# Kernel tuning notes

Measured on AMD Instinct MI355X. Metric: run time of the kernel, lower is better.

The kernel has to match this reference:

```python
import jax, jax.numpy as jnp
import numpy as np

N_NODES = 50000
N_EDGES = 800000
D_IN, D_HID, D_LAT = 128, 128, 64
BN_EPS = 1e-5


def setup_inputs() -> dict:
    key = jax.random.key(0)
    ks = jax.random.split(key, 8)
    x = jax.random.normal(ks[0], (N_NODES, D_IN), dtype=jnp.float32)
    edge_index = jax.random.randint(ks[1], (2, N_EDGES), 0, N_NODES, dtype=jnp.int64)
    s1 = 1.0 / np.sqrt(D_IN)
    s2 = 1.0 / np.sqrt(D_HID)
    W1 = jax.random.normal(ks[2], (D_IN, D_HID), dtype=jnp.float32) * s1
    b1 = jnp.zeros((D_HID,), jnp.float32)
    gamma = jnp.ones((D_HID,), jnp.float32)
    beta = jnp.zeros((D_HID,), jnp.float32)
    Wmu = jax.random.normal(ks[3], (D_HID, D_LAT), dtype=jnp.float32) * s2
    bmu = jnp.zeros((D_LAT,), jnp.float32)
    Wls = jax.random.normal(ks[4], (D_HID, D_LAT), dtype=jnp.float32) * s2
    bls = jnp.zeros((D_LAT,), jnp.float32)
    return {"x": x, "edge_index": edge_index, "W1": W1, "b1": b1,
            "gamma": gamma, "beta": beta, "Wmu": Wmu, "bmu": bmu,
            "Wls": Wls, "bls": bls}


def _gcn_conv(h, src, dst, norm_e, inv_deg, W, b):
    # PyG GCNConv: linear transform, then sym-normalized aggregation (A+I).
    h = h @ W                                   # [N, F]
    msgs = h[src] * norm_e[:, None]             # gather + edge scaling, [E, F]
    agg = jax.ops.segment_sum(msgs, dst, num_segments=h.shape[0])
    # self-loop contribution: norm[i]*norm[i] = 1/deg[i]
    return agg + h * inv_deg[:, None] + b


def reference(x, edge_index, W1, b1, gamma, beta, Wmu, bmu, Wls, bls):
    src, dst = edge_index[0], edge_index[1]
    n = x.shape[0]
    # degrees including self loops (GCN symmetric normalization)
    deg = jax.ops.segment_sum(jnp.ones(dst.shape, x.dtype), dst, num_segments=n) + 1.0
    inv_sqrt_deg = jax.lax.rsqrt(deg)
    norm_e = inv_sqrt_deg[src] * inv_sqrt_deg[dst]   # per-edge norm, [E]
    inv_deg = 1.0 / deg

    h = _gcn_conv(x, src, dst, norm_e, inv_deg, W1, b1)
    # BatchNorm1d with batch statistics (biased var), then ReLU; dropout off (eval)
    mean = h.mean(axis=0)
    var = h.var(axis=0)
    h = (h - mean) * jax.lax.rsqrt(var + BN_EPS) * gamma + beta
    h = jax.nn.relu(h)

    mu = _gcn_conv(h, src, dst, norm_e, inv_deg, Wmu, bmu)
    log_std = _gcn_conv(h, src, dst, norm_e, inv_deg, Wls, bls)
    return mu, log_std
```

## Files before the change

kernel.cpp:

```cpp
#include <hip/hip_runtime.h>
#include <hip/hip_bf16.h>

#define N_NODES 50000
#define N_EDGES 800000
#define F 128
#define L 64
#define BN_EPS 1e-5f
#define SCAN_BLOCKS 196
#define BN_BLOCKS 391
#define EDGE_BLOCKS 3125
#define GEMM_BLOCKS 782
#define NPART 8
#define PART_SZ 6250
#define SUBS 158
#define FILLB 1264

typedef __attribute__((ext_vector_type(8))) short short8;
typedef __attribute__((ext_vector_type(8))) unsigned short ushort8;
typedef __attribute__((ext_vector_type(4))) unsigned short ushortx4;
typedef __attribute__((ext_vector_type(4))) float f32x4;

static __device__ __forceinline__ float loadF(const void* p, int i, int f32) {
    if (f32) return ((const float*)p)[i];
    return __bfloat162float(((const __hip_bfloat16*)p)[i]);
}
static __device__ __forceinline__ float bfu2f(unsigned short u) {
    unsigned int t = ((unsigned int)u) << 16;
    float f;
    __builtin_memcpy(&f, &t, 4);
    return f;
}
static __device__ __forceinline__ short f2bf_s(float f) {
    union { __hip_bfloat16 b; short s; } cv;
    cv.b = __float2bfloat16(f);
    return cv.s;
}
static __device__ __forceinline__ unsigned short f2bf_u(float f) {
    union { __hip_bfloat16 b; unsigned short u; } cv;
    cv.b = __float2bfloat16(f);
    return cv.u;
}

__global__ void k_prep(const void* __restrict__ W1, const void* __restrict__ Wmu,
                       const void* __restrict__ Wls, const unsigned short* __restrict__ xs,
                       const void* __restrict__ ei, __hip_bfloat16* __restrict__ Wt1,
                       __hip_bfloat16* __restrict__ Wt2, int* __restrict__ flags,
                       int* __restrict__ degi, int* __restrict__ src32,
                       int* __restrict__ dst32, int* __restrict__ rank) {
    int b = blockIdx.x;
    int t = threadIdx.x;
    if (b == 0) {
        __shared__ int cnt[2];
        if (t < 2) cnt[t] = 0;
        __syncthreads();
        unsigned short v = xs[2 * t];
        int e = (v >> 7) & 0xff;
        int sane = (e >= 112 && e <= 133) ? 1 : 0;
        if (v == 0 || v == 0x8000) sane = 1;
        atomicAdd(&cnt[0], sane);
        atomicAdd(&cnt[1], (((const int*)ei)[2 * t + 1] != 0) ? 1 : 0);
        __syncthreads();
        if (t == 0) {
            flags[0] = (cnt[0] < 128) ? 1 : 0;
            flags[1] = (cnt[1] < 8) ? 1 : 0;
            flags[2] = 0;
        }
    } else if (b <= 64) {
        __shared__ int cnt;
        if (t == 0) cnt = 0;
        __syncthreads();
        unsigned short v = ((const unsigned short*)W1)[2 * t];
        int e = (v >> 7) & 0xff;
        atomicAdd(&cnt, (e >= 100 && e <= 133) ? 1 : 0);
        __syncthreads();
        int f32 = (cnt < 128) ? 1 : 0;
        int idx = (b - 1) * 256 + t;
        int n = idx >> 7, k = idx & 127;
        Wt1[idx] = __float2bfloat16(loadF(W1, k * F + n, f32));
        float v2 = (n < L) ? loadF(Wmu, k * L + n, f32) : loadF(Wls, k * L + (n - L), f32);
        Wt2[idx] = __float2bfloat16(v2);
    } else {
        int e0 = (b - 65) * 256 + t;
        __shared__ int nz;
        if (t == 0) nz = 0;
        __syncthreads();
        int w = ((const int*)ei)[2 * e0 + 1];
        if (w != 0) atomicAdd(&nz, 1);
        __syncthreads();
        int d;
        if (nz < 8) {
            int s = (int)((const long long*)ei)[e0];
            d = (int)((const long long*)ei)[N_EDGES + e0];
            src32[e0] = s;
            dst32[e0] = d;
        } else {
            d = ((const int*)ei)[N_EDGES + e0];
        }
        rank[e0] = atomicAdd(&degi[d], 1);
    }
}

__global__ void k_offs_alloc(const int* __restrict__ degi, int* __restrict__ flags,
                             int* __restrict__ offs, float* __restrict__ isd) {
    __shared__ int s[256];
    __shared__ int base;
    int t = threadIdx.x;
    int i = blockIdx.x * 256 + t;
    int v = (i < N_NODES) ? degi[i] : 0;
    s[t] = v;
    __syncthreads();
    for (int o = 1; o < 256; o <<= 1) {
        int u = (t >= o) ? s[t - o] : 0;
        __syncthreads();
        s[t] += u;
        __syncthreads();
    }
    if (t == 255) base = atomicAdd(&flags[2], s[255]);
    __syncthreads();
    if (i < N_NODES) {
        offs[i] = base + s[t] - v;
        isd[i] = 1.0f / sqrtf((float)v + 1.0f);
    }
}

static __device__ __forceinline__ void gemm_body(int bid, const void* __restrict__ Xin,
        const __hip_bfloat16* __restrict__ Wt, const float* __restrict__ isd,
        const int* __restrict__ flags, int mode,
        const float* __restrict__ bnscale, const float* __restrict__ bnshift,
        unsigned short* __restrict__ outb) {
    int wave = threadIdx.x >> 6, lane = threadIdx.x & 63;
    int quad = lane >> 4, mr = lane & 15;
    int m0 = bid * 64 + wave * 16;
    int node = m0 + mr;
    int row = (node < N_NODES) ? node : N_NODES - 1;
    short8 a[4];
    if (mode == 1) {
        const unsigned short* xb = (const unsigned short*)Xin;
#pragma unroll
        for (int t = 0; t < 4; ++t) {
            int k0 = t * 32 + quad * 8;
            ushort8 raw = *(const ushort8*)(xb + row * F + k0);
            f32x4 s0 = *(const f32x4*)(bnscale + k0);
            f32x4 s1 = *(const f32x4*)(bnscale + k0 + 4);
            f32x4 h0 = *(const f32x4*)(bnshift + k0);
            f32x4 h1 = *(const f32x4*)(bnshift + k0 + 4);
            short8 av;
#pragma unroll
            for (int j = 0; j < 4; ++j)
                av[j] = f2bf_s(fmaxf(bfu2f(raw[j]) * s0[j] + h0[j], 0.f));
#pragma unroll
            for (int j = 0; j < 4; ++j)
                av[4 + j] = f2bf_s(fmaxf(bfu2f(raw[4 + j]) * s1[j] + h1[j], 0.f));
            a[t] = av;
        }
    } else if (flags[0]) {
        const float* xf = (const float*)Xin;
#pragma unroll
        for (int t = 0; t < 4; ++t) {
            int off = row * F + t * 32 + quad * 8;
            f32x4 v0 = *(const f32x4*)(xf + off);
            f32x4 v1 = *(const f32x4*)(xf + off + 4);
            short8 av;
#pragma unroll
            for (int j = 0; j < 4; ++j) av[j] = f2bf_s(v0[j]);
#pragma unroll
            for (int j = 0; j < 4; ++j) av[4 + j] = f2bf_s(v1[j]);
            a[t] = av;
        }
    } else {
        const short* xb = (const short*)Xin;
#pragma unroll
        for (int t = 0; t < 4; ++t)
            a[t] = *(const short8*)(xb + row * F + t * 32 + quad * 8);
    }
    f32x4 acc[8];
    const short* wb = (const short*)Wt;
#pragma unroll
    for (int nt = 0; nt < 8; ++nt) {
        const short* wp = wb + (nt * 16 + mr) * F + quad * 8;
        f32x4 c = {0.f, 0.f, 0.f, 0.f};
        c = __builtin_amdgcn_mfma_f32_16x16x32_bf16(*(const short8*)(wp), a[0], c, 0, 0, 0);
        c = __builtin_amdgcn_mfma_f32_16x16x32_bf16(*(const short8*)(wp + 32), a[1], c, 0, 0, 0);
        c = __builtin_amdgcn_mfma_f32_16x16x32_bf16(*(const short8*)(wp + 64), a[2], c, 0, 0, 0);
        c = __builtin_amdgcn_mfma_f32_16x16x32_bf16(*(const short8*)(wp + 96), a[3], c, 0, 0, 0);
        acc[nt] = c;
    }
    if (node < N_NODES) {
        float sd = isd[node];
        unsigned short* op = outb + node * F;
#pragma unroll
        for (int nt = 0; nt < 8; ++nt) {
            ushortx4 r;
#pragma unroll
            for (int j = 0; j < 4; ++j) r[j] = f2bf_u(acc[nt][j] * sd);
            *(ushortx4*)(op + nt * 16 + quad * 4) = r;
        }
    }
}

__global__ __launch_bounds__(256) void k_fill_gemm1(
        const int* __restrict__ ei32, const int* __restrict__ src32,
        const int* __restrict__ dst32, const int* __restrict__ rank,
        const int* __restrict__ flags, const int* __restrict__ offs,
        int* __restrict__ csr,
        const void* __restrict__ X, const __hip_bfloat16* __restrict__ Wt1,
        const float* __restrict__ isd, unsigned short* __restrict__ outb) {
    if (blockIdx.x < GEMM_BLOCKS) {
        gemm_body(blockIdx.x, X, Wt1, isd, flags, 0, nullptr, nullptr, outb);
    } else {
        const int* sp;
        const int* dp;
        if (flags[1]) { sp = src32; dp = dst32; }
        else          { sp = ei32;  dp = ei32 + N_EDGES; }
        int grp = blockIdx.x & (NPART - 1);
        int sub = (blockIdx.x - GEMM_BLOCKS) >> 3;
        int lo = grp * PART_SZ, hi = lo + PART_SZ;
        int stride = SUBS * 256;
        for (int e = sub * 256 + threadIdx.x; e < N_EDGES; e += stride) {
            int d = dp[e];
            if (d >= lo && d < hi) csr[offs[d] + rank[e]] = sp[e];
        }
    }
}

__global__ __launch_bounds__(256) void k_gemm_bn(const void* __restrict__ Xin,
        const __hip_bfloat16* __restrict__ Wt, const float* __restrict__ isd,
        const int* __restrict__ flags, const float* __restrict__ bnscale,
        const float* __restrict__ bnshift, unsigned short* __restrict__ outb) {
    gemm_body(blockIdx.x, Xin, Wt, isd, flags, 1, bnscale, bnshift, outb);
}

static __device__ __forceinline__ void agg_accum(int node, int grp, int l16,
        const ushort8* __restrict__ vp, const int* __restrict__ csr,
        const int* __restrict__ offs, const int* __restrict__ degi, float acc[8]) {
#pragma unroll
    for (int j = 0; j < 8; ++j) acc[j] = 0.f;
    if (grp == 0) {
        ushort8 u = vp[node * 16 + l16];
#pragma unroll
        for (int j = 0; j < 8; ++j) acc[j] = bfu2f(u[j]);
    }
    int start = offs[node];
    int end = start + degi[node];
    int i = start + grp;
    for (; i + 12 < end; i += 16) {
        ushort8 u0 = vp[csr[i] * 16 + l16];
        ushort8 u1 = vp[csr[i + 4] * 16 + l16];
        ushort8 u2 = vp[csr[i + 8] * 16 + l16];
        ushort8 u3 = vp[csr[i + 12] * 16 + l16];
#pragma unroll
        for (int j = 0; j < 8; ++j)
            acc[j] += (bfu2f(u0[j]) + bfu2f(u1[j])) + (bfu2f(u2[j]) + bfu2f(u3[j]));
    }
    for (; i + 4 < end; i += 8) {
        ushort8 u0 = vp[csr[i] * 16 + l16];
        ushort8 u1 = vp[csr[i + 4] * 16 + l16];
#pragma unroll
        for (int j = 0; j < 8; ++j) acc[j] += bfu2f(u0[j]) + bfu2f(u1[j]);
    }
    for (; i < end; i += 4) {
        ushort8 u = vp[csr[i] * 16 + l16];
#pragma unroll
        for (int j = 0; j < 8; ++j) acc[j] += bfu2f(u[j]);
    }
#pragma unroll
    for (int j = 0; j < 8; ++j) {
        acc[j] += __shfl_xor(acc[j], 16);
        acc[j] += __shfl_xor(acc[j], 32);
    }
}

__global__ void k_agg1(const unsigned short* __restrict__ val, const int* __restrict__ csr,
                       const int* __restrict__ offs, const int* __restrict__ degi,
                       const float* __restrict__ isd, const void* __restrict__ b1,
                       const int* __restrict__ flags, unsigned short* __restrict__ out) {
    int node = blockIdx.x * 4 + (threadIdx.x >> 6);
    if (node >= N_NODES) return;
    int lane = threadIdx.x & 63;
    int grp = lane >> 4, l16 = lane & 15;
    float acc[8];
    agg_accum(node, grp, l16, (const ushort8*)val, csr, offs, degi, acc);
    if (grp == 0) {
        float sd = isd[node];
        int c0 = l16 * 8, f32 = flags[0];
        ushort8 r;
#pragma unroll
        for (int j = 0; j < 8; ++j) r[j] = f2bf_u(acc[j] * sd + loadF(b1, c0 + j, f32));
        ((ushort8*)out)[node * 16 + l16] = r;
    }
}

__global__ void k_bnstats(const unsigned short* __restrict__ h, float* __restrict__ partial) {
    __shared__ float ls[256][8];
    __shared__ float lq[256][8];
    int t = threadIdx.x;
    int o = t & 15, rg = t >> 4;
    int row0 = blockIdx.x * 128 + rg;
    float s[8] = {0.f}, q[8] = {0.f};
#pragma unroll
    for (int i = 0; i < 8; ++i) {
        int row = row0 + i * 16;
        if (row < N_NODES) {
            ushort8 u = *(const ushort8*)(h + row * F + o * 8);
#pragma unroll
            for (int j = 0; j < 8; ++j) {
                float v = bfu2f(u[j]);
                s[j] += v;
                q[j] += v * v;
            }
        }
    }
#pragma unroll
    for (int j = 0; j < 8; ++j) { ls[t][j] = s[j]; lq[t][j] = q[j]; }
    __syncthreads();
    if (t < 128) {
        int c = t, oo = c >> 3, jj = c & 7;
        float ts = 0.f, tq = 0.f;
#pragma unroll
        for (int rgi = 0; rgi < 16; ++rgi) {
            ts += ls[rgi * 16 + oo][jj];
            tq += lq[rgi * 16 + oo][jj];
        }
        partial[blockIdx.x * 256 + c] = ts;
        partial[blockIdx.x * 256 + 128 + c] = tq;
    }
}

__global__ void k_bnredprep(const float* __restrict__ partial, const void* __restrict__ gamma,
                            const void* __restrict__ beta, const int* __restrict__ flags,
                            float* __restrict__ scale, float* __restrict__ shift) {
    int c = blockIdx.x;
    float s = 0.f, q = 0.f;
    for (int b = threadIdx.x; b < BN_BLOCKS; b += 256) {
        s += partial[b * 256 + c];
        q += partial[b * 256 + 128 + c];
    }
#pragma unroll
    for (int o = 32; o; o >>= 1) {
        s += __shfl_down(s, o);
        q += __shfl_down(q, o);
    }
    __shared__ float ws[4], wq[4];
    if ((threadIdx.x & 63) == 0) {
        ws[threadIdx.x >> 6] = s;
        wq[threadIdx.x >> 6] = q;
    }
    __syncthreads();
    if (threadIdx.x == 0) {
        float S = ws[0] + ws[1] + ws[2] + ws[3];
        float Q = wq[0] + wq[1] + wq[2] + wq[3];
        const float invN = 1.0f / (float)N_NODES;
        float m = S * invN;
        float var = Q * invN - m * m;
        int f32 = flags[0];
        float sc = loadF(gamma, c, f32) * rsqrtf(var + BN_EPS);
        scale[c] = sc;
        shift[c] = loadF(beta, c, f32) - m * sc;
    }
}

__global__ void k_agg2(const unsigned short* __restrict__ val, const int* __restrict__ csr,
                       const int* __restrict__ offs, const int* __restrict__ degi,
                       const float* __restrict__ isd, const void* __restrict__ bmu,
                       const void* __restrict__ bls, const int* __restrict__ flags,
                       void* __restrict__ out) {
    int node = blockIdx.x * 4 + (threadIdx.x >> 6);
    if (node >= N_NODES) return;
    int lane = threadIdx.x & 63;
    int grp = lane >> 4, l16 = lane & 15;
    float acc[8];
    agg_accum(node, grp, l16, (const ushort8*)val, csr, offs, degi, acc);
    if (grp == 0) {
        float sd = isd[node];
        int c0 = l16 * 8, f32 = flags[0];
        int hsel = (c0 >= L) ? 1 : 0;
        int cc = c0 - hsel * L;
        const void* bp = hsel ? bls : bmu;
        float o8[8];
#pragma unroll
        for (int j = 0; j < 8; ++j) o8[j] = acc[j] * sd + loadF(bp, cc + j, f32);
        long base_o = (long)hsel * (N_NODES * 64) + (long)node * 64 + cc;
        if (f32) {
            f32x4 r0 = {o8[0], o8[1], o8[2], o8[3]};
            f32x4 r1 = {o8[4], o8[5], o8[6], o8[7]};
            __builtin_nontemporal_store(r0, (f32x4*)((float*)out + base_o));
            __builtin_nontemporal_store(r1, (f32x4*)((float*)out + base_o + 4));
        } else {
            ushort8 r;
#pragma unroll
            for (int j = 0; j < 8; ++j) r[j] = f2bf_u(o8[j]);
            __builtin_nontemporal_store(r, (ushort8*)((__hip_bfloat16*)out + base_o));
        }
    }
}

extern "C" void kernel_launch(void* const* d_in, const int* in_sizes, int n_in,
                              void* d_out, int out_size, void* d_ws, size_t ws_size,
                              hipStream_t stream) {
    const void* x     = d_in[0];
    const void* ei    = d_in[1];
    const void* W1    = d_in[2];
    const void* b1    = d_in[3];
    const void* gamma = d_in[4];
    const void* beta  = d_in[5];
    const void* Wmu   = d_in[6];
    const void* bmu   = d_in[7];
    const void* Wls   = d_in[8];
    const void* bls   = d_in[9];

    int*   degi  = (int*)d_ws;
    int*   offs  = degi + 50048;
    float* isd   = (float*)(offs + 50048);
    float* stats = isd + 50048;
    int*   flags = (int*)(stats + 512);
    int*   csr   = flags + 16;
    int*   src32 = csr + 800000;
    int*   dst32 = src32 + 800000;
    int*   rank  = dst32 + 800000;
    __hip_bfloat16* Wt1 = (__hip_bfloat16*)(rank + 800000);
    __hip_bfloat16* Wt2 = Wt1 + 16384;
    unsigned short* Abf = (unsigned short*)(Wt2 + 16384);
    unsigned short* Hpre = Abf + N_NODES * F;
    float* partial = (float*)(Hpre + N_NODES * F);

    const int NT = 256;
    const int AGG_BLOCKS = (N_NODES + 3) / 4;

    hipMemsetAsync(degi, 0, 50048 * sizeof(int), stream);
    k_prep<<<65 + EDGE_BLOCKS, NT, 0, stream>>>(W1, Wmu, Wls, (const unsigned short*)x,
                                                ei, Wt1, Wt2, flags, degi, src32, dst32,
                                                rank);
    k_offs_alloc<<<SCAN_BLOCKS, NT, 0, stream>>>(degi, flags, offs, isd);
    k_fill_gemm1<<<GEMM_BLOCKS + FILLB, NT, 0, stream>>>(
        (const int*)ei, src32, dst32, rank, flags, offs, csr, x, Wt1, isd, Abf);
    k_agg1<<<AGG_BLOCKS, NT, 0, stream>>>(Abf, csr, offs, degi, isd, b1, flags, Hpre);
    k_bnstats<<<BN_BLOCKS, NT, 0, stream>>>(Hpre, partial);
    k_bnredprep<<<128, NT, 0, stream>>>(partial, gamma, beta, flags, stats, stats + 128);
    k_gemm_bn<<<GEMM_BLOCKS, NT, 0, stream>>>(Hpre, Wt2, isd, flags, stats, stats + 128, Abf);
    k_agg2<<<AGG_BLOCKS, NT, 0, stream>>>(Abf, csr, offs, degi, isd, bmu, bls, flags, d_out);
}
```

Baseline: 286.4 us.

## Overlap GEMM1 with edge degree counting by moving source normalization into aggregation

The first GEMM no longer scales its output rows by the source node's inverse sqrt degree. That lets it run in the same launch as edge degree counting instead of waiting for the degree scan. The per-source scale moves into the aggregation loops, which now load isd[src] for every gathered neighbour and multiply per element. The CSR fill becomes its own kernel with more blocks. The cost is an extra gather per edge in both aggregations, plus one more kernel launch.

```diff
diff --git a/kernel.cpp b/kernel.cpp
--- a/kernel.cpp
+++ b/kernel.cpp
@@ -12,8 +12,8 @@
 #define GEMM_BLOCKS 782
 #define NPART 8
 #define PART_SZ 6250
-#define SUBS 158
-#define FILLB 1264
+#define SUBS_F 256
+#define FILLB_A 2048
 
 typedef __attribute__((ext_vector_type(8))) short short8;
 typedef __attribute__((ext_vector_type(8))) unsigned short ushort8;
@@ -41,12 +41,10 @@
     return cv.u;
 }
 
-__global__ void k_prep(const void* __restrict__ W1, const void* __restrict__ Wmu,
-                       const void* __restrict__ Wls, const unsigned short* __restrict__ xs,
-                       const void* __restrict__ ei, __hip_bfloat16* __restrict__ Wt1,
-                       __hip_bfloat16* __restrict__ Wt2, int* __restrict__ flags,
-                       int* __restrict__ degi, int* __restrict__ src32,
-                       int* __restrict__ dst32, int* __restrict__ rank) {
+__global__ void k_wprep(const void* __restrict__ W1, const void* __restrict__ Wmu,
+                        const void* __restrict__ Wls, const unsigned short* __restrict__ xs,
+                        const void* __restrict__ ei, __hip_bfloat16* __restrict__ Wt1,
+                        __hip_bfloat16* __restrict__ Wt2, int* __restrict__ flags) {
     int b = blockIdx.x;
     int t = threadIdx.x;
     if (b == 0) {
@@ -65,7 +63,7 @@
             flags[1] = (cnt[1] < 8) ? 1 : 0;
             flags[2] = 0;
         }
-    } else if (b <= 64) {
+    } else {
         __shared__ int cnt;
         if (t == 0) cnt = 0;
         __syncthreads();
@@ -79,8 +77,92 @@
         Wt1[idx] = __float2bfloat16(loadF(W1, k * F + n, f32));
         float v2 = (n < L) ? loadF(Wmu, k * L + n, f32) : loadF(Wls, k * L + (n - L), f32);
         Wt2[idx] = __float2bfloat16(v2);
+    }
+}
+
+static __device__ __forceinline__ void gemm_body(int bid, const void* __restrict__ Xin,
+        const __hip_bfloat16* __restrict__ Wt, const int* __restrict__ flags, int mode,
+        const float* __restrict__ bnscale, const float* __restrict__ bnshift,
+        unsigned short* __restrict__ outb) {
+    int wave = threadIdx.x >> 6, lane = threadIdx.x & 63;
+    int quad = lane >> 4, mr = lane & 15;
+    int m0 = bid * 64 + wave * 16;
+    int node = m0 + mr;
+    int row = (node < N_NODES) ? node : N_NODES - 1;
+    short8 a[4];
+    if (mode == 1) {
+        const unsigned short* xb = (const unsigned short*)Xin;
+#pragma unroll
+        for (int t = 0; t < 4; ++t) {
+            int k0 = t * 32 + quad * 8;
+            ushort8 raw = *(const ushort8*)(xb + row * F + k0);
+            f32x4 s0 = *(const f32x4*)(bnscale + k0);
+            f32x4 s1 = *(const f32x4*)(bnscale + k0 + 4);
+            f32x4 h0 = *(const f32x4*)(bnshift + k0);
+            f32x4 h1 = *(const f32x4*)(bnshift + k0 + 4);
+            short8 av;
+#pragma unroll
+            for (int j = 0; j < 4; ++j)
+                av[j] = f2bf_s(fmaxf(bfu2f(raw[j]) * s0[j] + h0[j], 0.f));
+#pragma unroll
+            for (int j = 0; j < 4; ++j)
+                av[4 + j] = f2bf_s(fmaxf(bfu2f(raw[4 + j]) * s1[j] + h1[j], 0.f));
+            a[t] = av;
+        }
+    } else if (flags[0]) {
+        const float* xf = (const float*)Xin;
+#pragma unroll
+        for (int t = 0; t < 4; ++t) {
+            int off = row * F + t * 32 + quad * 8;
+            f32x4 v0 = *(const f32x4*)(xf + off);
+            f32x4 v1 = *(const f32x4*)(xf + off + 4);
+            short8 av;
+#pragma unroll
+            for (int j = 0; j < 4; ++j) av[j] = f2bf_s(v0[j]);
+#pragma unroll
+            for (int j = 0; j < 4; ++j) av[4 + j] = f2bf_s(v1[j]);
+            a[t] = av;
+        }
     } else {
-        int e0 = (b - 65) * 256 + t;
+        const short* xb = (const short*)Xin;
+#pragma unroll
+        for (int t = 0; t < 4; ++t)
+            a[t] = *(const short8*)(xb + row * F + t * 32 + quad * 8);
+    }
+    f32x4 acc[8];
+    const short* wb = (const short*)Wt;
+#pragma unroll
+    for (int nt = 0; nt < 8; ++nt) {
+        const short* wp = wb + (nt * 16 + mr) * F + quad * 8;
+        f32x4 c = {0.f, 0.f, 0.f, 0.f};
+        c = __builtin_amdgcn_mfma_f32_16x16x32_bf16(*(const short8*)(wp), a[0], c, 0, 0, 0);
+        c = __builtin_amdgcn_mfma_f32_16x16x32_bf16(*(const short8*)(wp + 32), a[1], c, 0, 0, 0);
+        c = __builtin_amdgcn_mfma_f32_16x16x32_bf16(*(const short8*)(wp + 64), a[2], c, 0, 0, 0);
+        c = __builtin_amdgcn_mfma_f32_16x16x32_bf16(*(const short8*)(wp + 96), a[3], c, 0, 0, 0);
+        acc[nt] = c;
+    }
+    if (node < N_NODES) {
+        unsigned short* op = outb + node * F;
+#pragma unroll
+        for (int nt = 0; nt < 8; ++nt) {
+            ushortx4 r;
+#pragma unroll
+            for (int j = 0; j < 4; ++j) r[j] = f2bf_u(acc[nt][j]);
+            *(ushortx4*)(op + nt * 16 + quad * 4) = r;
+        }
+    }
+}
+
+__global__ __launch_bounds__(256) void k_edge_gemm1(
+        const void* __restrict__ X, const __hip_bfloat16* __restrict__ Wt1,
+        const int* __restrict__ flags, const void* __restrict__ ei,
+        int* __restrict__ degi, int* __restrict__ src32, int* __restrict__ dst32,
+        int* __restrict__ rank, unsigned short* __restrict__ outb) {
+    if (blockIdx.x < GEMM_BLOCKS) {
+        gemm_body(blockIdx.x, X, Wt1, flags, 0, nullptr, nullptr, outb);
+    } else {
+        int t = threadIdx.x;
+        int e0 = (blockIdx.x - GEMM_BLOCKS) * 256 + t;
         __shared__ int nz;
         if (t == 0) nz = 0;
         __syncthreads();
@@ -123,145 +205,73 @@
     }
 }
 
-static __device__ __forceinline__ void gemm_body(int bid, const void* __restrict__ Xin,
-        const __hip_bfloat16* __restrict__ Wt, const float* __restrict__ isd,
-        const int* __restrict__ flags, int mode,
-        const float* __restrict__ bnscale, const float* __restrict__ bnshift,
-        unsigned short* __restrict__ outb) {
-    int wave = threadIdx.x >> 6, lane = threadIdx.x & 63;
-    int quad = lane >> 4, mr = lane & 15;
-    int m0 = bid * 64 + wave * 16;
-    int node = m0 + mr;
-    int row = (node < N_NODES) ? node : N_NODES - 1;
-    short8 a[4];
-    if (mode == 1) {
-        const unsigned short* xb = (const unsigned short*)Xin;
-#pragma unroll
-        for (int t = 0; t < 4; ++t) {
-            int k0 = t * 32 + quad * 8;
-            ushort8 raw = *(const ushort8*)(xb + row * F + k0);
-            f32x4 s0 = *(const f32x4*)(bnscale + k0);
-            f32x4 s1 = *(const f32x4*)(bnscale + k0 + 4);
-            f32x4 h0 = *(const f32x4*)(bnshift + k0);
-            f32x4 h1 = *(const f32x4*)(bnshift + k0 + 4);
-            short8 av;
-#pragma unroll
-            for (int j = 0; j < 4; ++j)
-                av[j] = f2bf_s(fmaxf(bfu2f(raw[j]) * s0[j] + h0[j], 0.f));
-#pragma unroll
-            for (int j = 0; j < 4; ++j)
-                av[4 + j] = f2bf_s(fmaxf(bfu2f(raw[4 + j]) * s1[j] + h1[j], 0.f));
-            a[t] = av;
-        }
-    } else if (flags[0]) {
-        const float* xf = (const float*)Xin;
-#pragma unroll
-        for (int t = 0; t < 4; ++t) {
-            int off = row * F + t * 32 + quad * 8;
-            f32x4 v0 = *(const f32x4*)(xf + off);
-            f32x4 v1 = *(const f32x4*)(xf + off + 4);
-            short8 av;
-#pragma unroll
-            for (int j = 0; j < 4; ++j) av[j] = f2bf_s(v0[j]);
-#pragma unroll
-            for (int j = 0; j < 4; ++j) av[4 + j] = f2bf_s(v1[j]);
-            a[t] = av;
-        }
-    } else {
-        const short* xb = (const short*)Xin;
-#pragma unroll
-        for (int t = 0; t < 4; ++t)
-            a[t] = *(const short8*)(xb + row * F + t * 32 + quad * 8);
-    }
-    f32x4 acc[8];
-    const short* wb = (const short*)Wt;
-#pragma unroll
-    for (int nt = 0; nt < 8; ++nt) {
-        const short* wp = wb + (nt * 16 + mr) * F + quad * 8;
-        f32x4 c = {0.f, 0.f, 0.f, 0.f};
-        c = __builtin_amdgcn_mfma_f32_16x16x32_bf16(*(const short8*)(wp), a[0], c, 0, 0, 0);
-        c = __builtin_amdgcn_mfma_f32_16x16x32_bf16(*(const short8*)(wp + 32), a[1], c, 0, 0, 0);
-        c = __builtin_amdgcn_mfma_f32_16x16x32_bf16(*(const short8*)(wp + 64), a[2], c, 0, 0, 0);
-        c = __builtin_amdgcn_mfma_f32_16x16x32_bf16(*(const short8*)(wp + 96), a[3], c, 0, 0, 0);
-        acc[nt] = c;
-    }
-    if (node < N_NODES) {
-        float sd = isd[node];
-        unsigned short* op = outb + node * F;
-#pragma unroll
-        for (int nt = 0; nt < 8; ++nt) {
-            ushortx4 r;
-#pragma unroll
-            for (int j = 0; j < 4; ++j) r[j] = f2bf_u(acc[nt][j] * sd);
-            *(ushortx4*)(op + nt * 16 + quad * 4) = r;
-        }
-    }
-}
-
-__global__ __launch_bounds__(256) void k_fill_gemm1(
+__global__ __launch_bounds__(256) void k_fill(
         const int* __restrict__ ei32, const int* __restrict__ src32,
         const int* __restrict__ dst32, const int* __restrict__ rank,
         const int* __restrict__ flags, const int* __restrict__ offs,
-        int* __restrict__ csr,
-        const void* __restrict__ X, const __hip_bfloat16* __restrict__ Wt1,
-        const float* __restrict__ isd, unsigned short* __restrict__ outb) {
-    if (blockIdx.x < GEMM_BLOCKS) {
-        gemm_body(blockIdx.x, X, Wt1, isd, flags, 0, nullptr, nullptr, outb);
-    } else {
-        const int* sp;
-        const int* dp;
-        if (flags[1]) { sp = src32; dp = dst32; }
-        else          { sp = ei32;  dp = ei32 + N_EDGES; }
-        int grp = blockIdx.x & (NPART - 1);
-        int sub = (blockIdx.x - GEMM_BLOCKS) >> 3;
-        int lo = grp * PART_SZ, hi = lo + PART_SZ;
-        int stride = SUBS * 256;
-        for (int e = sub * 256 + threadIdx.x; e < N_EDGES; e += stride) {
-            int d = dp[e];
-            if (d >= lo && d < hi) csr[offs[d] + rank[e]] = sp[e];
-        }
+        int* __restrict__ csr) {
+    const int* sp;
+    const int* dp;
+    if (flags[1]) { sp = src32; dp = dst32; }
+    else          { sp = ei32;  dp = ei32 + N_EDGES; }
+    int grp = blockIdx.x & (NPART - 1);
+    int sub = blockIdx.x >> 3;
+    int lo = grp * PART_SZ, hi = lo + PART_SZ;
+    int stride = SUBS_F * 256;
+    for (int e = sub * 256 + threadIdx.x; e < N_EDGES; e += stride) {
+        int d = dp[e];
+        if (d >= lo && d < hi) csr[offs[d] + rank[e]] = sp[e];
     }
 }
 
 __global__ __launch_bounds__(256) void k_gemm_bn(const void* __restrict__ Xin,
-        const __hip_bfloat16* __restrict__ Wt, const float* __restrict__ isd,
-        const int* __restrict__ flags, const float* __restrict__ bnscale,
-        const float* __restrict__ bnshift, unsigned short* __restrict__ outb) {
-    gemm_body(blockIdx.x, Xin, Wt, isd, flags, 1, bnscale, bnshift, outb);
+        const __hip_bfloat16* __restrict__ Wt, const int* __restrict__ flags,
+        const float* __restrict__ bnscale, const float* __restrict__ bnshift,
+        unsigned short* __restrict__ outb) {
+    gemm_body(blockIdx.x, Xin, Wt, flags, 1, bnscale, bnshift, outb);
 }
 
 static __device__ __forceinline__ void agg_accum(int node, int grp, int l16,
         const ushort8* __restrict__ vp, const int* __restrict__ csr,
-        const int* __restrict__ offs, const int* __restrict__ degi, float acc[8]) {
+        const int* __restrict__ offs, const int* __restrict__ degi,
+        const float* __restrict__ isd, float acc[8]) {
 #pragma unroll
     for (int j = 0; j < 8; ++j) acc[j] = 0.f;
     if (grp == 0) {
+        float w = isd[node];
         ushort8 u = vp[node * 16 + l16];
 #pragma unroll
-        for (int j = 0; j < 8; ++j) acc[j] = bfu2f(u[j]);
+        for (int j = 0; j < 8; ++j) acc[j] = bfu2f(u[j]) * w;
     }
     int start = offs[node];
     int end = start + degi[node];
     int i = start + grp;
     for (; i + 12 < end; i += 16) {
-        ushort8 u0 = vp[csr[i] * 16 + l16];
-        ushort8 u1 = vp[csr[i + 4] * 16 + l16];
-        ushort8 u2 = vp[csr[i + 8] * 16 + l16];
-        ushort8 u3 = vp[csr[i + 12] * 16 + l16];
+        int s0 = csr[i], s1 = csr[i + 4], s2 = csr[i + 8], s3 = csr[i + 12];
+        float w0 = isd[s0], w1 = isd[s1], w2 = isd[s2], w3 = isd[s3];
+        ushort8 u0 = vp[s0 * 16 + l16];
+        ushort8 u1 = vp[s1 * 16 + l16];
+        ushort8 u2 = vp[s2 * 16 + l16];
+        ushort8 u3 = vp[s3 * 16 + l16];
 #pragma unroll
         for (int j = 0; j < 8; ++j)
-            acc[j] += (bfu2f(u0[j]) + bfu2f(u1[j])) + (bfu2f(u2[j]) + bfu2f(u3[j]));
+            acc[j] += (bfu2f(u0[j]) * w0 + bfu2f(u1[j]) * w1) +
+                      (bfu2f(u2[j]) * w2 + bfu2f(u3[j]) * w3);
     }
     for (; i + 4 < end; i += 8) {
-        ushort8 u0 = vp[csr[i] * 16 + l16];
-        ushort8 u1 = vp[csr[i + 4] * 16 + l16];
-#pragma unroll
-        for (int j = 0; j < 8; ++j) acc[j] += bfu2f(u0[j]) + bfu2f(u1[j]);
+        int s0 = csr[i], s1 = csr[i + 4];
+        float w0 = isd[s0], w1 = isd[s1];
+        ushort8 u0 = vp[s0 * 16 + l16];
+        ushort8 u1 = vp[s1 * 16 + l16];
+#pragma unroll
+        for (int j = 0; j < 8; ++j) acc[j] += bfu2f(u0[j]) * w0 + bfu2f(u1[j]) * w1;
     }
     for (; i < end; i += 4) {
-        ushort8 u = vp[csr[i] * 16 + l16];
-#pragma unroll
-        for (int j = 0; j < 8; ++j) acc[j] += bfu2f(u[j]);
+        int s0 = csr[i];
+        float w0 = isd[s0];
+        ushort8 u = vp[s0 * 16 + l16];
+#pragma unroll
+        for (int j = 0; j < 8; ++j) acc[j] += bfu2f(u[j]) * w0;
     }
 #pragma unroll
     for (int j = 0; j < 8; ++j) {
@@ -279,7 +289,7 @@
     int lane = threadIdx.x & 63;
     int grp = lane >> 4, l16 = lane & 15;
     float acc[8];
-    agg_accum(node, grp, l16, (const ushort8*)val, csr, offs, degi, acc);
+    agg_accum(node, grp, l16, (const ushort8*)val, csr, offs, degi, isd, acc);
     if (grp == 0) {
         float sd = isd[node];
         int c0 = l16 * 8, f32 = flags[0];
@@ -369,7 +379,7 @@
     int lane = threadIdx.x & 63;
     int grp = lane >> 4, l16 = lane & 15;
     float acc[8];
-    agg_accum(node, grp, l16, (const ushort8*)val, csr, offs, degi, acc);
+    agg_accum(node, grp, l16, (const ushort8*)val, csr, offs, degi, isd, acc);
     if (grp == 0) {
         float sd = isd[node];
         int c0 = l16 * 8, f32 = flags[0];
@@ -427,15 +437,16 @@
     const int AGG_BLOCKS = (N_NODES + 3) / 4;
 
     hipMemsetAsync(degi, 0, 50048 * sizeof(int), stream);
-    k_prep<<<65 + EDGE_BLOCKS, NT, 0, stream>>>(W1, Wmu, Wls, (const unsigned short*)x,
-                                                ei, Wt1, Wt2, flags, degi, src32, dst32,
-                                                rank);
+    k_wprep<<<65, NT, 0, stream>>>(W1, Wmu, Wls, (const unsigned short*)x, ei,
+                                   Wt1, Wt2, flags);
+    k_edge_gemm1<<<GEMM_BLOCKS + EDGE_BLOCKS, NT, 0, stream>>>(
+        x, Wt1, flags, ei, degi, src32, dst32, rank, Abf);
     k_offs_alloc<<<SCAN_BLOCKS, NT, 0, stream>>>(degi, flags, offs, isd);
-    k_fill_gemm1<<<GEMM_BLOCKS + FILLB, NT, 0, stream>>>(
-        (const int*)ei, src32, dst32, rank, flags, offs, csr, x, Wt1, isd, Abf);
+    k_fill<<<FILLB_A, NT, 0, stream>>>((const int*)ei, src32, dst32, rank,
+                                       flags, offs, csr);
     k_agg1<<<AGG_BLOCKS, NT, 0, stream>>>(Abf, csr, offs, degi, isd, b1, flags, Hpre);
     k_bnstats<<<BN_BLOCKS, NT, 0, stream>>>(Hpre, partial);
     k_bnredprep<<<128, NT, 0, stream>>>(partial, gamma, beta, flags, stats, stats + 128);
-    k_gemm_bn<<<GEMM_BLOCKS, NT, 0, stream>>>(Hpre, Wt2, isd, flags, stats, stats + 128, Abf);
+    k_gemm_bn<<<GEMM_BLOCKS, NT, 0, stream>>>(Hpre, Wt2, flags, stats, stats + 128, Abf);
     k_agg2<<<AGG_BLOCKS, NT, 0, stream>>>(Abf, csr, offs, degi, isd, bmu, bls, flags, d_out);
 }
```

Result: faster. 274.1 us (-4.3%).
